# Optimization experiments

Hardware: AMD Instinct MI355X
Metric: run time of the kernel (lower is better)

Reference implementation:

```python
import jax, jax.numpy as jnp
import numpy as np


def setup_inputs() -> dict:
    key = jax.random.key(0)
    k1, k2, k3, k4 = jax.random.split(key, 4)
    B, S, D = 8, 2048, 1024
    x = jax.random.normal(k1, (B, S, D), dtype=jnp.float32)
    scale = 1.0 / np.sqrt(D)  # glorot-ish magnitude
    Wq = jax.random.normal(k2, (D, D), dtype=jnp.float32) * scale
    Wk = jax.random.normal(k3, (D, D), dtype=jnp.float32) * scale
    Wv = jax.random.normal(k4, (D, D), dtype=jnp.float32) * scale
    return {"x": x, "Wq": Wq, "Wk": Wk, "Wv": Wv}


def reference(x, Wq, Wk, Wv):
    # q,k,v: [B,S,D]
    q = jnp.einsum("bsd,de->bse", x, Wq)
    k = jnp.einsum("bsd,de->bse", x, Wk)
    v = jnp.einsum("bsd,de->bse", x, Wv)
    d = k.shape[-1]
    # scores: [B,S,S], scaled by sqrt(d)
    scores = jnp.einsum("bqd,bkd->bqk", q, k) / jnp.sqrt(jnp.asarray(d, x.dtype))
    attn = jax.nn.softmax(scores, axis=-1)
    out = jnp.einsum("bqk,bkd->bqd", attn, v)
    return out
```

## Files before the change

### kernel.cpp

```cpp
#include <hip/hip_runtime.h>
#include <hip/hip_bf16.h>

typedef __bf16 bf16x8 __attribute__((ext_vector_type(8)));
typedef float  f32x4  __attribute__((ext_vector_type(4)));

static __device__ __forceinline__ unsigned short f2bf(float f) {
  unsigned int u = __float_as_uint(f);
  u += 0x7FFFu + ((u >> 16) & 1u);
  return (unsigned short)(u >> 16);
}

static __device__ __forceinline__ void gl_lds16(const void* g, void* l) {
  __builtin_amdgcn_global_load_lds(
      (const __attribute__((address_space(1))) void*)g,
      (__attribute__((address_space(3))) void*)l,
      16, 0, 0);
}

__global__ __launch_bounds__(256) void cast_f32_bf16(
    const float* __restrict__ in, unsigned short* __restrict__ out, int n) {
  int i = (blockIdx.x * 256 + threadIdx.x) * 4;
  const int stride = gridDim.x * 256 * 4;
  for (; i < n; i += stride) {
    float4 f = *(const float4*)(in + i);
    ushort4 o;
    o.x = f2bf(f.x); o.y = f2bf(f.y); o.z = f2bf(f.z); o.w = f2bf(f.w);
    *(ushort4*)(out + i) = o;
  }
}

__global__ __launch_bounds__(256) void transpose_cast_w(
    const float* __restrict__ w, unsigned short* __restrict__ wt) {
  __shared__ float tile[16][17];
  const int tx = threadIdx.x & 15, ty = threadIdx.x >> 4;
  const int bx = blockIdx.x * 16, by = blockIdx.y * 16;
  tile[ty][tx] = w[(size_t)(by + ty) * 1024 + bx + tx];
  __syncthreads();
  wt[(size_t)(bx + ty) * 1024 + by + tx] = f2bf(tile[tx][ty]);
}

template <int MODE>
__global__ __launch_bounds__(256, 2) void gemm_bt(
    const unsigned short* __restrict__ A, int lda, size_t astride,
    const unsigned short* __restrict__ B, int ldb, size_t bstride,
    int K, void* __restrict__ Cv, int ldc, size_t cstride,
    float* __restrict__ aux) {
  __shared__ __align__(16) unsigned char lds[32768];
  const unsigned d2 = blockIdx.x + gridDim.x * blockIdx.y;
  const unsigned ty = d2 % gridDim.y;
  const unsigned tx = d2 / gridDim.y;
  const int bn0 = tx * 128;
  const int bm0 = ty * 128;
  A += (size_t)blockIdx.z * astride;
  B += (size_t)blockIdx.z * bstride;

  const int tid = threadIdx.x;
  const int wid = tid >> 6, lane = tid & 63;
  const int wr = wid >> 1, wc = wid & 1;
  const int l15 = lane & 15, kq = lane >> 4;

  const int sr = tid >> 2;
  const int ssub = (tid & 3) * 8;
  size_t aoff[4], boff[4];
#pragma unroll
  for (int j = 0; j < 4; ++j) {
    const int r = (j & 1) * 64 + sr;
    const int kko = (j >> 1) * 32;
    aoff[j] = (size_t)(bm0 + r) * lda + kko + ssub;
    boff[j] = (size_t)(bn0 + r) * ldb + kko + ssub;
  }
  unsigned char* dstA = lds + wid * 1024;
  unsigned char* dstB = lds + 16384 + wid * 1024;

  f32x4 acc[4][4] = {};
  const int nkt = K >> 6;
  for (int kt = 0; kt < nkt; ++kt) {
    const int kc = kt << 6;
#pragma unroll
    for (int j = 0; j < 4; ++j) {
      gl_lds16(A + aoff[j] + kc, dstA + j * 4096);
      gl_lds16(B + boff[j] + kc, dstB + j * 4096);
    }
    __syncthreads();

#pragma unroll
    for (int kk = 0; kk < 2; ++kk) {
      bf16x8 af[4], bg[4];
#pragma unroll
      for (int mi = 0; mi < 4; ++mi)
        af[mi] = *(const bf16x8*)(lds + kk * 8192 + (wr * 64 + mi * 16 + l15) * 64 + kq * 16);
#pragma unroll
      for (int ni = 0; ni < 4; ++ni)
        bg[ni] = *(const bf16x8*)(lds + 16384 + kk * 8192 + (wc * 64 + ni * 16 + l15) * 64 + kq * 16);
#pragma unroll
      for (int mi = 0; mi < 4; ++mi)
#pragma unroll
        for (int ni = 0; ni < 4; ++ni)
          acc[mi][ni] = __builtin_amdgcn_mfma_f32_16x16x32_bf16(af[mi], bg[ni], acc[mi][ni], 0, 0, 0);
    }
    __syncthreads();
  }

  if constexpr (MODE == 3) {
#pragma unroll
    for (int mi = 0; mi < 4; ++mi)
#pragma unroll
      for (int ni = 0; ni < 4; ++ni)
#pragma unroll
        for (int r = 0; r < 4; ++r) {
          const int row = bm0 + wr * 64 + mi * 16 + kq * 4 + r;
          const int col = bn0 + wc * 64 + ni * 16 + l15;
          const float v = acc[mi][ni][r];
          unsigned short* q = (unsigned short*)Cv;
          if (col < 1024) {
            q[(size_t)row * 1024 + col] = f2bf(v);
          } else if (col < 2048) {
            q[16777216u + (size_t)row * 1024 + (col - 1024)] = f2bf(v);
          } else {
            const int b = row >> 11, s = row & 2047;
            q[33554432u + ((size_t)(b * 1024 + (col - 2048))) * 2048 + s] = f2bf(v);
          }
        }
  } else if constexpr (MODE == 4) {
    __shared__ float redsm[128][2];
    unsigned short* pp = (unsigned short*)Cv + (size_t)blockIdx.z * cstride;
    float rs[4][4];
#pragma unroll
    for (int mi = 0; mi < 4; ++mi)
#pragma unroll
      for (int r = 0; r < 4; ++r) rs[mi][r] = 0.f;
#pragma unroll
    for (int mi = 0; mi < 4; ++mi)
#pragma unroll
      for (int ni = 0; ni < 4; ++ni)
#pragma unroll
        for (int r = 0; r < 4; ++r) {
          const float e = exp2f(acc[mi][ni][r] * 0.045084220027780106f);
          rs[mi][r] += e;
          const int row = bm0 + wr * 64 + mi * 16 + kq * 4 + r;
          const int col = bn0 + wc * 64 + ni * 16 + l15;
          pp[(size_t)row * ldc + col] = f2bf(e);
        }
#pragma unroll
    for (int mi = 0; mi < 4; ++mi)
#pragma unroll
      for (int r = 0; r < 4; ++r) {
        float s = rs[mi][r];
        s += __shfl_xor(s, 1); s += __shfl_xor(s, 2);
        s += __shfl_xor(s, 4); s += __shfl_xor(s, 8);
        rs[mi][r] = s;
      }
    if (l15 == 0) {
#pragma unroll
      for (int mi = 0; mi < 4; ++mi)
#pragma unroll
        for (int r = 0; r < 4; ++r)
          redsm[wr * 64 + mi * 16 + kq * 4 + r][wc] = rs[mi][r];
    }
    __syncthreads();
    if (tid < 128)
      aux[((size_t)blockIdx.z * 16 + tx) * 2048 + bm0 + tid] =
          redsm[tid][0] + redsm[tid][1];
  } else {
    const float* inv = aux + (size_t)blockIdx.z * 2048;
    float* op = (float*)Cv + (size_t)blockIdx.z * cstride;
#pragma unroll
    for (int mi = 0; mi < 4; ++mi)
#pragma unroll
      for (int r = 0; r < 4; ++r) {
        const int row = bm0 + wr * 64 + mi * 16 + kq * 4 + r;
        const float iv = inv[row];
#pragma unroll
        for (int ni = 0; ni < 4; ++ni) {
          const int col = bn0 + wc * 64 + ni * 16 + l15;
          op[(size_t)row * ldc + col] = acc[mi][ni][r] * iv;
        }
      }
  }
}

__global__ __launch_bounds__(256) void combine_inv(
    const float* __restrict__ part, float* __restrict__ inv, int n) {
  const int i = blockIdx.x * 256 + threadIdx.x;
  if (i >= n) return;
  const int z = i >> 11, row = i & 2047;
  const float* p = part + ((size_t)z * 16) * 2048 + row;
  float s = 0.f;
#pragma unroll
  for (int j = 0; j < 16; ++j) s += p[j * 2048];
  inv[i] = 1.0f / s;
}

extern "C" void kernel_launch(void* const* d_in, const int* in_sizes, int n_in,
                              void* d_out, int out_size, void* d_ws, size_t ws_size,
                              hipStream_t stream) {
  const float* x  = (const float*)d_in[0];
  const float* Wq = (const float*)d_in[1];
  const float* Wk = (const float*)d_in[2];
  const float* Wv = (const float*)d_in[3];
  float* out = (float*)d_out;
  char* ws = (char*)d_ws;

  unsigned short* xb     = (unsigned short*)ws;
  unsigned short* wt_all = (unsigned short*)(ws + 33554432);
  unsigned short* qb     = (unsigned short*)(ws + 39845888);
  unsigned short* kb     = qb + 16777216;
  unsigned short* vt     = kb + 16777216;
  const size_t off_scores = 140509184ull;

  const size_t per_b = 8388608ull + 131072ull + 8192ull;
  int G; char *pPc, *partc, *invc;
  const size_t avail = ws_size > off_scores ? ws_size - off_scores : 0;
  G = (int)(avail / per_b); if (G > 8) G = 8;
  if (G >= 1) {
    pPc   = ws + off_scores;
    partc = pPc + (size_t)G * 8388608ull;
    invc  = partc + (size_t)G * 131072ull;
  } else {
    G = 2;
    pPc   = ws;
    partc = ws + 2 * 8388608ull;
    invc  = partc + 2 * 131072ull;
  }

  cast_f32_bf16<<<2048, 256, 0, stream>>>(x, xb, 16384 * 1024);
  transpose_cast_w<<<dim3(64, 64), 256, 0, stream>>>(Wq, wt_all);
  transpose_cast_w<<<dim3(64, 64), 256, 0, stream>>>(Wk, wt_all + 1048576);
  transpose_cast_w<<<dim3(64, 64), 256, 0, stream>>>(Wv, wt_all + 2097152);

  gemm_bt<3><<<dim3(24, 128), 256, 0, stream>>>(xb, 1024, 0, wt_all, 1024, 0,
                                                1024, qb, 0, 0, nullptr);

  for (int b0 = 0; b0 < 8; b0 += G) {
    const int g = (8 - b0) < G ? (8 - b0) : G;
    const size_t so = (size_t)b0 * 2097152;
    gemm_bt<4><<<dim3(16, 16, g), 256, 0, stream>>>(
        qb + so, 1024, 2097152, kb + so, 1024, 2097152, 1024,
        (unsigned short*)pPc, 2048, 4194304, (float*)partc);
    combine_inv<<<(g * 2048 + 255) / 256, 256, 0, stream>>>(
        (const float*)partc, (float*)invc, g * 2048);
    gemm_bt<5><<<dim3(8, 16, g), 256, 0, stream>>>(
        (const unsigned short*)pPc, 2048, 4194304,
        vt + so, 2048, 2097152, 2048,
        out + so, 1024, 2097152, (float*)invc);
  }
}
```

Measured before the change: 346.2 us.

## Double-buffer GEMM LDS staging to overlap global loads with MFMA compute

Doubles the LDS tile buffer so the next K-tile's global_load_lds is issued before computing on the current one, with a single barrier per iteration instead of two. Fragment reads use inline ds_read_b128 with explicit waitcnt, and the MFMA block runs under raised wave priority. This is meant to hide global-memory latency behind matrix math. The cost is 64KB of LDS per block, which may cut occupancy below the two blocks per CU the launch bounds ask for, and hand-written waitcnt sequencing is fragile.

```diff
diff --git a/kernel.cpp b/kernel.cpp
--- a/kernel.cpp
+++ b/kernel.cpp
@@ -45,7 +45,7 @@
     const unsigned short* __restrict__ B, int ldb, size_t bstride,
     int K, void* __restrict__ Cv, int ldc, size_t cstride,
     float* __restrict__ aux) {
-  __shared__ __align__(16) unsigned char lds[32768];
+  __shared__ __align__(16) unsigned char lds[65536];
   const unsigned d2 = blockIdx.x + gridDim.x * blockIdx.y;
   const unsigned ty = d2 % gridDim.y;
   const unsigned tx = d2 / gridDim.y;
@@ -69,37 +69,59 @@
     aoff[j] = (size_t)(bm0 + r) * lda + kko + ssub;
     boff[j] = (size_t)(bn0 + r) * ldb + kko + ssub;
   }
-  unsigned char* dstA = lds + wid * 1024;
-  unsigned char* dstB = lds + 16384 + wid * 1024;
+
+#define STAGE(t) do { \
+    unsigned char* bufA_ = lds + ((t) & 1) * 32768 + wid * 1024; \
+    unsigned char* bufB_ = bufA_ + 16384; \
+    const int kc_ = (t) << 6; \
+    _Pragma("unroll") \
+    for (int j = 0; j < 4; ++j) { \
+      gl_lds16(A + aoff[j] + kc_, bufA_ + j * 4096); \
+      gl_lds16(B + boff[j] + kc_, bufB_ + j * 4096); \
+    } \
+  } while (0)
+#define DSR(dst, addr) asm volatile("ds_read_b128 %0, %1" : "=v"(dst) : "v"(addr))
+
+  const unsigned ldsbase =
+      (unsigned)(unsigned long long)(__attribute__((address_space(3))) unsigned char*)lds;
+  const unsigned aA = ldsbase + (wr * 64 + l15) * 64 + kq * 16;
+  const unsigned aB = ldsbase + 16384 + (wc * 64 + l15) * 64 + kq * 16;
 
   f32x4 acc[4][4] = {};
   const int nkt = K >> 6;
-  for (int kt = 0; kt < nkt; ++kt) {
-    const int kc = kt << 6;
-#pragma unroll
-    for (int j = 0; j < 4; ++j) {
-      gl_lds16(A + aoff[j] + kc, dstA + j * 4096);
-      gl_lds16(B + boff[j] + kc, dstB + j * 4096);
+
+  STAGE(0);
+  asm volatile("s_waitcnt vmcnt(0)" ::: "memory");
+  __builtin_amdgcn_s_barrier();
+
+  for (int t = 0; t < nkt; ++t) {
+    if (t + 1 < nkt) STAGE(t + 1);
+    const unsigned bofs = (unsigned)(t & 1) * 32768u;
+
+    bf16x8 af[2][4], bg[2][4];
+#pragma unroll
+    for (int kk = 0; kk < 2; ++kk) {
+#pragma unroll
+      for (int mi = 0; mi < 4; ++mi) DSR(af[kk][mi], bofs + aA + kk * 8192 + mi * 1024);
+#pragma unroll
+      for (int ni = 0; ni < 4; ++ni) DSR(bg[kk][ni], bofs + aB + kk * 8192 + ni * 1024);
     }
-    __syncthreads();
-
-#pragma unroll
-    for (int kk = 0; kk < 2; ++kk) {
-      bf16x8 af[4], bg[4];
+    asm volatile("s_waitcnt lgkmcnt(0)" ::: "memory");
+    __builtin_amdgcn_sched_barrier(0);
+    __builtin_amdgcn_s_setprio(1);
+#pragma unroll
+    for (int kk = 0; kk < 2; ++kk)
 #pragma unroll
       for (int mi = 0; mi < 4; ++mi)
-        af[mi] = *(const bf16x8*)(lds + kk * 8192 + (wr * 64 + mi * 16 + l15) * 64 + kq * 16);
-#pragma unroll
-      for (int ni = 0; ni < 4; ++ni)
-        bg[ni] = *(const bf16x8*)(lds + 16384 + kk * 8192 + (wc * 64 + ni * 16 + l15) * 64 + kq * 16);
-#pragma unroll
-      for (int mi = 0; mi < 4; ++mi)
 #pragma unroll
         for (int ni = 0; ni < 4; ++ni)
-          acc[mi][ni] = __builtin_amdgcn_mfma_f32_16x16x32_bf16(af[mi], bg[ni], acc[mi][ni], 0, 0, 0);
-    }
-    __syncthreads();
-  }
+          acc[mi][ni] = __builtin_amdgcn_mfma_f32_16x16x32_bf16(af[kk][mi], bg[kk][ni], acc[mi][ni], 0, 0, 0);
+    __builtin_amdgcn_s_setprio(0);
+    asm volatile("s_waitcnt vmcnt(0)" ::: "memory");
+    __builtin_amdgcn_s_barrier();
+  }
+#undef STAGE
+#undef DSR
 
   if constexpr (MODE == 3) {
 #pragma unroll
```

After: 367.5 us. 6.2% more time.
